# Kernel optimization log

Measured on AMD Instinct MI355X. Metric: run time of the kernel, lower is better.

## Reference

```python
import jax, jax.numpy as jnp
import numpy as np

N_NODES = 100000
N_EDGES = 1600000
N_GRAPHS = 2000
N_FEAT = 128
HIDDEN = 128
N_LAYERS = 4
BN_EPS = 1e-5


def setup_inputs() -> dict:
    key = jax.random.key(0)
    ks = jax.random.split(key, 8)
    x = jax.random.normal(ks[0], (N_NODES, N_FEAT), dtype=jnp.float32)
    edge_index = jax.random.randint(ks[1], (2, N_EDGES), 0, N_NODES, dtype=jnp.int32)
    batch = jnp.sort(jax.random.randint(ks[2], (N_NODES,), 0, N_GRAPHS, dtype=jnp.int32))
    # layer weights scaled down to keep activations stable over 4 layers
    Ws = jax.random.normal(ks[3], (N_LAYERS, HIDDEN, HIDDEN), dtype=jnp.float32) * 0.1
    bs = jnp.zeros((N_LAYERS, HIDDEN), jnp.float32)
    gammas = jnp.ones((N_LAYERS, HIDDEN), jnp.float32)
    betas = jnp.zeros((N_LAYERS, HIDDEN), jnp.float32)
    run_mean = jnp.zeros((N_LAYERS, HIDDEN), jnp.float32)
    run_var = jnp.ones((N_LAYERS, HIDDEN), jnp.float32)
    W_out = jax.random.normal(ks[4], (HIDDEN, 5), dtype=jnp.float32) * 0.1
    b_out = jnp.zeros((5,), jnp.float32)
    return {"x": x, "edge_index": edge_index, "batch": batch, "Ws": Ws, "bs": bs,
            "gammas": gammas, "betas": betas, "run_mean": run_mean, "run_var": run_var,
            "W_out": W_out, "b_out": b_out}


def _gcn_conv(x, src, dst, norm, self_coef, W, b):
    xw = x @ W                                        # [N, H]
    coef = norm[src] * norm[dst]                      # [E]
    msgs = xw[src] * coef[:, None]                    # [E, H] gather
    agg = jax.ops.segment_sum(msgs, dst, num_segments=N_NODES)  # scatter-add
    agg = agg + xw * self_coef[:, None]               # self-loop term
    return agg + b


def reference(x, edge_index, batch, Ws, bs, gammas, betas, run_mean, run_var, W_out, b_out):
    src, dst = edge_index[0], edge_index[1]
    # degree (incl. self-loop) from destination index
    deg = jax.ops.segment_sum(jnp.ones((N_EDGES,), x.dtype), dst, num_segments=N_NODES) + 1.0
    norm = jax.lax.rsqrt(deg)
    self_coef = norm * norm
    h = x
    for l in range(N_LAYERS):
        h = _gcn_conv(h, src, dst, norm, self_coef, Ws[l], bs[l])
        # BatchNorm1d in eval mode (running stats); dropout is identity in eval
        h = (h - run_mean[l]) * (gammas[l] * jax.lax.rsqrt(run_var[l] + BN_EPS)) + betas[l]
        h = jax.nn.relu(h)
    # global mean pool over graphs
    sums = jax.ops.segment_sum(h, batch, num_segments=N_GRAPHS)
    counts = jax.ops.segment_sum(jnp.ones((N_NODES,), h.dtype), batch, num_segments=N_GRAPHS)
    pooled = sums / jnp.maximum(counts, 1.0)[:, None]  # [G, H]
    return pooled @ W_out + b_out                      # [G, 5]
```

## Files before the change

kernel.cpp:

```cpp
#include <hip/hip_runtime.h>
#include <hip/hip_fp16.h>

#define N_NODES_C 100000
#define N_EDGES_C 1600000
#define N_GRAPHS_C 2000
#define HID 128
#define BN_EPS_C 1e-5f
#define NBUCK 391
#define PART_TILE 4096

typedef _Float16 half8 __attribute__((ext_vector_type(8)));
typedef float float4v __attribute__((ext_vector_type(4)));


__global__ __launch_bounds__(256) void kb_hist(const int* __restrict__ dst, int* __restrict__ bcount) {
    __shared__ int hist[NBUCK];
    const int t = threadIdx.x;
    for (int b = t; b < NBUCK; b += 256) hist[b] = 0;
    __syncthreads();
    const int e0 = blockIdx.x * PART_TILE;
    #pragma unroll
    for (int k = 0; k < 16; k++) {
        int e = e0 + k * 256 + t;
        if (e < N_EDGES_C) atomicAdd(&hist[dst[e] >> 8], 1);
    }
    __syncthreads();
    for (int b = t; b < NBUCK; b += 256) {
        int c = hist[b];
        if (c) atomicAdd(&bcount[b], c);
    }
}

__global__ __launch_bounds__(512) void kb_scan(const int* __restrict__ bcount,
                                               int* __restrict__ bbase, int* __restrict__ bcursor) {
    __shared__ int s[512];
    const int t = threadIdx.x;
    int v = (t < NBUCK) ? bcount[t] : 0;
    s[t] = v;
    __syncthreads();
    for (int off = 1; off < 512; off <<= 1) {
        int u = (t >= off) ? s[t - off] : 0;
        __syncthreads();
        s[t] += u;
        __syncthreads();
    }
    if (t < NBUCK) { int e = s[t] - v; bbase[t] = e; bcursor[t] = e; }
    if (t == 0) bbase[NBUCK] = N_EDGES_C;
}

__global__ __launch_bounds__(256) void kb_part(const int* __restrict__ src, const int* __restrict__ dst,
                                               int* __restrict__ bcursor, int2* __restrict__ ebuf) {
    __shared__ int hist[NBUCK];
    __shared__ int startA[NBUCK];
    __shared__ int lcur[NBUCK];
    const int t = threadIdx.x;
    for (int b = t; b < NBUCK; b += 256) { hist[b] = 0; lcur[b] = 0; }
    __syncthreads();
    const int e0 = blockIdx.x * PART_TILE;
    #pragma unroll
    for (int k = 0; k < 16; k++) {
        int e = e0 + k * 256 + t;
        if (e < N_EDGES_C) atomicAdd(&hist[dst[e] >> 8], 1);
    }
    __syncthreads();
    for (int b = t; b < NBUCK; b += 256) {
        int c = hist[b];
        startA[b] = c ? atomicAdd(&bcursor[b], c) : 0;
    }
    __syncthreads();
    #pragma unroll
    for (int k = 0; k < 16; k++) {
        int e = e0 + k * 256 + t;
        if (e < N_EDGES_C) {
            int d = dst[e];
            int b = d >> 8;
            int pos = startA[b] + atomicAdd(&lcur[b], 1);
            ebuf[pos] = make_int2(src[e], d);
        }
    }
}

__global__ __launch_bounds__(256) void kb_fill(const int2* __restrict__ ebuf, const int* __restrict__ bbase,
                                               int* __restrict__ csr_src, int* __restrict__ offs,
                                               float* __restrict__ norm) {
    __shared__ int s[256];
    __shared__ int excl[256];
    __shared__ int lcur[256];
    const int b = blockIdx.x, t = threadIdx.x;
    const int base = b << 8;
    const int e0 = bbase[b], e1 = bbase[b + 1];
    s[t] = 0; lcur[t] = 0;
    __syncthreads();
    for (int e = e0 + t; e < e1; e += 256)
        atomicAdd(&s[ebuf[e].y & 255], 1);
    __syncthreads();
    int own = s[t];
    for (int off = 1; off < 256; off <<= 1) {
        int v = (t >= off) ? s[t - off] : 0;
        __syncthreads();
        s[t] += v;
        __syncthreads();
    }
    excl[t] = s[t] - own;
    int node = base + t;
    if (node < N_NODES_C) {
        offs[node] = e0 + (s[t] - own);
        norm[node] = rsqrtf((float)own + 1.0f);
    }
    if (b == 0 && t == 0) offs[N_NODES_C] = N_EDGES_C;
    __syncthreads();
    for (int e = e0 + t; e < e1; e += 256) {
        int2 p = ebuf[e];
        int l = p.y & 255;
        int pos = e0 + excl[l] + atomicAdd(&lcur[l], 1);
        csr_src[pos] = p.x;
    }
}


__global__ __launch_bounds__(256) void k_cast(const float* __restrict__ x, _Float16* __restrict__ xh) {
    long i = ((long)blockIdx.x * 256 + threadIdx.x) * 8;
    float4 a = *(const float4*)&x[i];
    float4 b = *(const float4*)&x[i + 4];
    _Float16 p[8] = {(_Float16)a.x, (_Float16)a.y, (_Float16)a.z, (_Float16)a.w,
                     (_Float16)b.x, (_Float16)b.y, (_Float16)b.z, (_Float16)b.w};
    *(half8*)&xh[i] = *(half8*)p;
}

__global__ __launch_bounds__(256) void k_tw(const float* __restrict__ Ws_all, _Float16* __restrict__ WT) {
    int idx = blockIdx.x * 256 + threadIdx.x;
    int l = idx >> 14, r = idx & 16383, k = r >> 7, n = r & 127;
    WT[l * 16384 + n * HID + k] = (_Float16)Ws_all[idx];
}


__global__ __launch_bounds__(256) void k_gemm(const _Float16* __restrict__ Ah,
                                              const _Float16* __restrict__ WT,
                                              const float* __restrict__ norm,
                                              _Float16* __restrict__ Y, int nrows) {
    __shared__ _Float16 Wt[HID][136];
    const int tid = threadIdx.x;
    #pragma unroll
    for (int t = 0; t < 8; t++) {
        int off = tid * 8 + t * 2048;
        half8 v = *(const half8*)&WT[off];
        *(half8*)&Wt[off >> 7][off & 127] = v;
    }
    __syncthreads();

    const int wave = tid >> 6, lane = tid & 63, quad = lane >> 4, l16 = lane & 15;
    half8 Wf[2][4];
    #pragma unroll
    for (int c = 0; c < 2; c++)
        #pragma unroll
        for (int ks = 0; ks < 4; ks++)
            Wf[c][ks] = *(const half8*)&Wt[(wave * 2 + c) * 16 + l16][ks * 32 + quad * 8];

    const int nbase = blockIdx.x * 128;
    #pragma unroll
    for (int t = 0; t < 8; t++) {
        int node = nbase + t * 16 + l16;
        bool ok = node < nrows;
        half8 Af[4];
        const _Float16* arow = Ah + (long)node * HID;
        #pragma unroll
        for (int ks = 0; ks < 4; ks++)
            Af[ks] = ok ? *(const half8*)&arow[ks * 32 + quad * 8] : half8{};
        float4v a0 = {0.f, 0.f, 0.f, 0.f}, a1 = {0.f, 0.f, 0.f, 0.f};
        #pragma unroll
        for (int ks = 0; ks < 4; ks++) {
            a0 = __builtin_amdgcn_mfma_f32_16x16x32_f16(Wf[0][ks], Af[ks], a0, 0, 0, 0);
            a1 = __builtin_amdgcn_mfma_f32_16x16x32_f16(Wf[1][ks], Af[ks], a1, 0, 0, 0);
        }
        if (ok) {
            float nv = norm[node];
            _Float16 p0[4], p1[4];
            #pragma unroll
            for (int r = 0; r < 4; r++) {
                p0[r] = (_Float16)(a0[r] * nv);
                p1[r] = (_Float16)(a1[r] * nv);
            }
            *(ushort4*)&Y[(long)node * HID + (wave * 2 + 0) * 16 + quad * 4] = *(ushort4*)p0;
            *(ushort4*)&Y[(long)node * HID + (wave * 2 + 1) * 16 + quad * 4] = *(ushort4*)p1;
        }
    }
}


__global__ __launch_bounds__(256) void k_agg(const __half* __restrict__ y, const int* __restrict__ offs,
                                             const int* __restrict__ csr_src, const float* __restrict__ norm,
                                             const float* __restrict__ bias, const float* __restrict__ mean,
                                             const float* __restrict__ gamma, const float* __restrict__ var,
                                             const float* __restrict__ beta, __half* __restrict__ h) {
    const int wave = __builtin_amdgcn_readfirstlane(threadIdx.x >> 6);
    const int lane = threadIdx.x & 63;
    const int i = blockIdx.x * 4 + wave;
    const int j = lane * 2;

    float2 f = __half22float2(*(const __half2*)&y[(long)i * HID + j]);
    float acc0 = f.x, acc1 = f.y;

    const int e0 = offs[i], e1 = offs[i + 1];
    int e = e0;
    #define GATHER(EE) { \
        int s_ = csr_src[EE]; \
        float2 g_ = __half22float2(*(const __half2*)&y[(long)s_ * HID + j]); \
        acc0 += g_.x; acc1 += g_.y; }
    for (; e + 8 <= e1; e += 8) {
        GATHER(e) GATHER(e + 1) GATHER(e + 2) GATHER(e + 3)
        GATHER(e + 4) GATHER(e + 5) GATHER(e + 6) GATHER(e + 7)
    }
    for (; e < e1; e++) GATHER(e)
    #undef GATHER

    float ni = norm[i];
    float2 bi = *(const float2*)&bias[j];
    float2 me = *(const float2*)&mean[j];
    float2 ga = *(const float2*)&gamma[j];
    float2 va = *(const float2*)&var[j];
    float2 be = *(const float2*)&beta[j];
    float v0 = (acc0 * ni + bi.x - me.x) * (ga.x * rsqrtf(va.x + BN_EPS_C)) + be.x;
    float v1 = (acc1 * ni + bi.y - me.y) * (ga.y * rsqrtf(va.y + BN_EPS_C)) + be.y;
    *(__half2*)&h[(long)i * HID + j] = __floats2half2_rn(fmaxf(v0, 0.f), fmaxf(v1, 0.f));
}


__global__ __launch_bounds__(128) void k_pool(const __half* __restrict__ h, const int* __restrict__ batch,
                                              float* __restrict__ psum, int* __restrict__ pcount) {
    const int j = threadIdx.x;
    const int i0 = blockIdx.x * 128;
    const int iend = min(i0 + 128, N_NODES_C);
    if (i0 >= N_NODES_C) return;
    float acc = 0.f;
    int cur = batch[i0];
    int runStart = i0;
    for (int i = i0; i < iend; i++) {
        int g = batch[i];
        if (g != cur) {
            atomicAdd(&psum[(long)cur * HID + j], acc);
            if (j == 0) atomicAdd(&pcount[cur], i - runStart);
            acc = 0.f; cur = g; runStart = i;
        }
        acc += __half2float(h[(long)i * HID + j]);
    }
    atomicAdd(&psum[(long)cur * HID + j], acc);
    if (j == 0) atomicAdd(&pcount[cur], iend - runStart);
}

__global__ __launch_bounds__(128) void k_final(const float* __restrict__ psum, const int* __restrict__ pcount,
                                               const float* __restrict__ W_out, const float* __restrict__ b_out,
                                               float* __restrict__ out) {
    __shared__ float red[128][5];
    const int g = blockIdx.x, j = threadIdx.x;
    float cnt = fmaxf((float)pcount[g], 1.f);
    float p = psum[(long)g * HID + j] / cnt;
    #pragma unroll
    for (int o = 0; o < 5; o++) red[j][o] = p * W_out[j * 5 + o];
    __syncthreads();
    for (int off = 64; off >= 1; off >>= 1) {
        if (j < off) {
            #pragma unroll
            for (int o = 0; o < 5; o++) red[j][o] += red[j + off][o];
        }
        __syncthreads();
    }
    if (j < 5) out[g * 5 + j] = red[0][j] + b_out[j];
}


extern "C" void kernel_launch(void* const* d_in, const int* in_sizes, int n_in,
                              void* d_out, int out_size, void* d_ws, size_t ws_size,
                              hipStream_t stream) {
    const float* x        = (const float*)d_in[0];
    const int*   eidx     = (const int*)d_in[1];
    const int*   src      = eidx;
    const int*   dst      = eidx + N_EDGES_C;
    const int*   batch    = (const int*)d_in[2];
    const float* Ws_all   = (const float*)d_in[3];
    const float* bs       = (const float*)d_in[4];
    const float* gammas   = (const float*)d_in[5];
    const float* betas    = (const float*)d_in[6];
    const float* run_mean = (const float*)d_in[7];
    const float* run_var  = (const float*)d_in[8];
    const float* W_out    = (const float*)d_in[9];
    const float* b_out    = (const float*)d_in[10];
    float* out = (float*)d_out;

    char* wp = (char*)d_ws;
    auto alloc = [&](size_t bytes) { char* p = wp; wp += (bytes + 255) & ~(size_t)255; return p; };
    __half*   h       = (__half*)alloc((size_t)N_NODES_C * HID * 2);
    _Float16* y       = (_Float16*)alloc((size_t)N_NODES_C * HID * 2);
    int2*     ebuf    = (int2*)y;
    _Float16* xh      = (_Float16*)alloc((size_t)N_NODES_C * HID * 2);
    _Float16* WT      = (_Float16*)alloc((size_t)4 * HID * HID * 2);
    int*      csr_src = (int*)alloc((size_t)N_EDGES_C * 4);
    int*      offs    = (int*)alloc((size_t)(N_NODES_C + 1) * 4);
    float*    norm    = (float*)alloc((size_t)N_NODES_C * 4);
    int*      bcount  = (int*)alloc((NBUCK + 1) * 4);
    int*      bbase   = (int*)alloc((NBUCK + 1) * 4);
    int*      bcursor = (int*)alloc((NBUCK + 1) * 4);
    float*    psum    = (float*)alloc((size_t)N_GRAPHS_C * HID * 4);
    int*      pcount  = (int*)alloc((size_t)N_GRAPHS_C * 4);

    hipMemsetAsync(bcount, 0, (NBUCK + 1) * 4, stream);
    hipMemsetAsync(psum,   0, (size_t)N_GRAPHS_C * HID * 4, stream);
    hipMemsetAsync(pcount, 0, (size_t)N_GRAPHS_C * 4, stream);

    k_cast<<<(N_NODES_C * HID) / 2048, 256, 0, stream>>>(x, xh);
    k_tw  <<<256, 256, 0, stream>>>(Ws_all, WT);

    const int PB = (N_EDGES_C + PART_TILE - 1) / PART_TILE;
    kb_hist<<<PB, 256, 0, stream>>>(dst, bcount);
    kb_scan<<<1, 512, 0, stream>>>(bcount, bbase, bcursor);
    kb_part<<<PB, 256, 0, stream>>>(src, dst, bcursor, ebuf);
    kb_fill<<<NBUCK, 256, 0, stream>>>(ebuf, bbase, csr_src, offs, norm);

    const int GB = (N_NODES_C + 127) / 128;
    const int AB = (N_NODES_C + 3) / 4;
    for (int l = 0; l < 4; l++) {
        const _Float16* A = (l == 0) ? xh : (const _Float16*)h;
        k_gemm<<<GB, 256, 0, stream>>>(A, WT + (size_t)l * HID * HID, norm, y, N_NODES_C);
        k_agg<<<AB, 256, 0, stream>>>((const __half*)y, offs, csr_src, norm,
                                      bs + l * HID, run_mean + l * HID, gammas + l * HID,
                                      run_var + l * HID, betas + l * HID, h);
    }
    k_pool <<<GB, 128, 0, stream>>>(h, batch, psum, pcount);
    k_final<<<N_GRAPHS_C, 128, 0, stream>>>(psum, pcount, W_out, b_out, out);
}
```

Before: 555.5 us.

## Widen aggregation gathers, pack edge buffer, precompute BN affine, drop GEMM LDS staging

The aggregation kernel now has each 16-lane group load a full 16-byte half8 chunk per neighbor, with four edges handled in parallel per wave and combined by cross-lane shuffles. This replaces per-lane 4-byte gathers and is meant to cut memory transactions on the dominant gather. The edge partition buffer packs src and the low dst bits into one 32-bit word, halving that traffic. BatchNorm scale and shift are precomputed once per layer in a tiny kernel. The GEMM reads weights straight from global memory instead of staging them in LDS, and the pool kernel processes two columns per thread.

New measurement: 568.9 us. +2.4%, slower.

```diff
diff --git a/kernel.cpp b/kernel.cpp
--- a/kernel.cpp
+++ b/kernel.cpp
@@ -49,7 +49,7 @@
 }
 
 __global__ __launch_bounds__(256) void kb_part(const int* __restrict__ src, const int* __restrict__ dst,
-                                               int* __restrict__ bcursor, int2* __restrict__ ebuf) {
+                                               int* __restrict__ bcursor, unsigned int* __restrict__ ebuf) {
     __shared__ int hist[NBUCK];
     __shared__ int startA[NBUCK];
     __shared__ int lcur[NBUCK];
@@ -75,12 +75,12 @@
             int d = dst[e];
             int b = d >> 8;
             int pos = startA[b] + atomicAdd(&lcur[b], 1);
-            ebuf[pos] = make_int2(src[e], d);
-        }
-    }
-}
-
-__global__ __launch_bounds__(256) void kb_fill(const int2* __restrict__ ebuf, const int* __restrict__ bbase,
+            ebuf[pos] = ((unsigned int)src[e] << 8) | (unsigned int)(d & 255);
+        }
+    }
+}
+
+__global__ __launch_bounds__(256) void kb_fill(const unsigned int* __restrict__ ebuf, const int* __restrict__ bbase,
                                                int* __restrict__ csr_src, int* __restrict__ offs,
                                                float* __restrict__ norm) {
     __shared__ int s[256];
@@ -92,7 +92,7 @@
     s[t] = 0; lcur[t] = 0;
     __syncthreads();
     for (int e = e0 + t; e < e1; e += 256)
-        atomicAdd(&s[ebuf[e].y & 255], 1);
+        atomicAdd(&s[ebuf[e] & 255u], 1);
     __syncthreads();
     int own = s[t];
     for (int off = 1; off < 256; off <<= 1) {
@@ -110,21 +110,21 @@
     if (b == 0 && t == 0) offs[N_NODES_C] = N_EDGES_C;
     __syncthreads();
     for (int e = e0 + t; e < e1; e += 256) {
-        int2 p = ebuf[e];
-        int l = p.y & 255;
+        unsigned int p = ebuf[e];
+        int l = p & 255u;
         int pos = e0 + excl[l] + atomicAdd(&lcur[l], 1);
-        csr_src[pos] = p.x;
+        csr_src[pos] = (int)(p >> 8);
     }
 }
 
 
 __global__ __launch_bounds__(256) void k_cast(const float* __restrict__ x, _Float16* __restrict__ xh) {
-    long i = ((long)blockIdx.x * 256 + threadIdx.x) * 8;
-    float4 a = *(const float4*)&x[i];
-    float4 b = *(const float4*)&x[i + 4];
+    long base = ((long)blockIdx.x * 256 + threadIdx.x) * 8;
+    float4 a = *(const float4*)&x[base];
+    float4 b = *(const float4*)&x[base + 4];
     _Float16 p[8] = {(_Float16)a.x, (_Float16)a.y, (_Float16)a.z, (_Float16)a.w,
                      (_Float16)b.x, (_Float16)b.y, (_Float16)b.z, (_Float16)b.w};
-    *(half8*)&xh[i] = *(half8*)p;
+    *(half8*)&xh[base] = *(half8*)p;
 }
 
 __global__ __launch_bounds__(256) void k_tw(const float* __restrict__ Ws_all, _Float16* __restrict__ WT) {
@@ -133,28 +133,32 @@
     WT[l * 16384 + n * HID + k] = (_Float16)Ws_all[idx];
 }
 
+__global__ __launch_bounds__(256) void k_bn(const float* __restrict__ bs, const float* __restrict__ mean,
+                                            const float* __restrict__ gamma, const float* __restrict__ var,
+                                            const float* __restrict__ beta,
+                                            float* __restrict__ Asc, float* __restrict__ Bsh) {
+    int i = blockIdx.x * 256 + threadIdx.x;
+    if (i < 4 * HID) {
+        float sc = gamma[i] * rsqrtf(var[i] + BN_EPS_C);
+        Asc[i] = sc;
+        Bsh[i] = (bs[i] - mean[i]) * sc + beta[i];
+    }
+}
+
 
 __global__ __launch_bounds__(256) void k_gemm(const _Float16* __restrict__ Ah,
                                               const _Float16* __restrict__ WT,
                                               const float* __restrict__ norm,
                                               _Float16* __restrict__ Y, int nrows) {
-    __shared__ _Float16 Wt[HID][136];
     const int tid = threadIdx.x;
-    #pragma unroll
-    for (int t = 0; t < 8; t++) {
-        int off = tid * 8 + t * 2048;
-        half8 v = *(const half8*)&WT[off];
-        *(half8*)&Wt[off >> 7][off & 127] = v;
-    }
-    __syncthreads();
-
     const int wave = tid >> 6, lane = tid & 63, quad = lane >> 4, l16 = lane & 15;
+
     half8 Wf[2][4];
     #pragma unroll
     for (int c = 0; c < 2; c++)
         #pragma unroll
         for (int ks = 0; ks < 4; ks++)
-            Wf[c][ks] = *(const half8*)&Wt[(wave * 2 + c) * 16 + l16][ks * 32 + quad * 8];
+            Wf[c][ks] = *(const half8*)&WT[((wave * 2 + c) * 16 + l16) * HID + ks * 32 + quad * 8];
 
     const int nbase = blockIdx.x * 128;
     #pragma unroll
@@ -187,63 +191,98 @@
 }
 
 
-__global__ __launch_bounds__(256) void k_agg(const __half* __restrict__ y, const int* __restrict__ offs,
+__global__ __launch_bounds__(256) void k_agg(const _Float16* __restrict__ y, const int* __restrict__ offs,
                                              const int* __restrict__ csr_src, const float* __restrict__ norm,
-                                             const float* __restrict__ bias, const float* __restrict__ mean,
-                                             const float* __restrict__ gamma, const float* __restrict__ var,
-                                             const float* __restrict__ beta, __half* __restrict__ h) {
-    const int wave = __builtin_amdgcn_readfirstlane(threadIdx.x >> 6);
+                                             const float* __restrict__ Asc, const float* __restrict__ Bsh,
+                                             _Float16* __restrict__ h) {
+    const int wave = threadIdx.x >> 6;
     const int lane = threadIdx.x & 63;
+    const int q = lane >> 4, cl = lane & 15;
     const int i = blockIdx.x * 4 + wave;
-    const int j = lane * 2;
-
-    float2 f = __half22float2(*(const __half2*)&y[(long)i * HID + j]);
-    float acc0 = f.x, acc1 = f.y;
+
+    float acc[8] = {0.f, 0.f, 0.f, 0.f, 0.f, 0.f, 0.f, 0.f};
+    if (q == 0) {
+        half8 sv = *(const half8*)&y[(long)i * HID + cl * 8];
+        #pragma unroll
+        for (int r = 0; r < 8; r++) acc[r] += (float)sv[r];
+    }
 
     const int e0 = offs[i], e1 = offs[i + 1];
     int e = e0;
-    #define GATHER(EE) { \
-        int s_ = csr_src[EE]; \
-        float2 g_ = __half22float2(*(const __half2*)&y[(long)s_ * HID + j]); \
-        acc0 += g_.x; acc1 += g_.y; }
-    for (; e + 8 <= e1; e += 8) {
-        GATHER(e) GATHER(e + 1) GATHER(e + 2) GATHER(e + 3)
-        GATHER(e + 4) GATHER(e + 5) GATHER(e + 6) GATHER(e + 7)
-    }
-    for (; e < e1; e++) GATHER(e)
-    #undef GATHER
-
-    float ni = norm[i];
-    float2 bi = *(const float2*)&bias[j];
-    float2 me = *(const float2*)&mean[j];
-    float2 ga = *(const float2*)&gamma[j];
-    float2 va = *(const float2*)&var[j];
-    float2 be = *(const float2*)&beta[j];
-    float v0 = (acc0 * ni + bi.x - me.x) * (ga.x * rsqrtf(va.x + BN_EPS_C)) + be.x;
-    float v1 = (acc1 * ni + bi.y - me.y) * (ga.y * rsqrtf(va.y + BN_EPS_C)) + be.y;
-    *(__half2*)&h[(long)i * HID + j] = __floats2half2_rn(fmaxf(v0, 0.f), fmaxf(v1, 0.f));
-}
-
-
-__global__ __launch_bounds__(128) void k_pool(const __half* __restrict__ h, const int* __restrict__ batch,
-                                              float* __restrict__ psum, int* __restrict__ pcount) {
+    for (; e + 16 <= e1; e += 16) {
+        int s0 = csr_src[e + q];
+        int s1 = csr_src[e + 4 + q];
+        int s2 = csr_src[e + 8 + q];
+        int s3 = csr_src[e + 12 + q];
+        half8 v0 = *(const half8*)&y[(long)s0 * HID + cl * 8];
+        half8 v1 = *(const half8*)&y[(long)s1 * HID + cl * 8];
+        half8 v2 = *(const half8*)&y[(long)s2 * HID + cl * 8];
+        half8 v3 = *(const half8*)&y[(long)s3 * HID + cl * 8];
+        #pragma unroll
+        for (int r = 0; r < 8; r++)
+            acc[r] += (float)v0[r] + (float)v1[r] + (float)v2[r] + (float)v3[r];
+    }
+    for (; e + 4 <= e1; e += 4) {
+        int s = csr_src[e + q];
+        half8 v = *(const half8*)&y[(long)s * HID + cl * 8];
+        #pragma unroll
+        for (int r = 0; r < 8; r++) acc[r] += (float)v[r];
+    }
+    if (e + q < e1) {
+        int s = csr_src[e + q];
+        half8 v = *(const half8*)&y[(long)s * HID + cl * 8];
+        #pragma unroll
+        for (int r = 0; r < 8; r++) acc[r] += (float)v[r];
+    }
+
+    #pragma unroll
+    for (int r = 0; r < 8; r++) {
+        acc[r] += __shfl_xor(acc[r], 16);
+        acc[r] += __shfl_xor(acc[r], 32);
+    }
+
+    if (q == 0) {
+        float ni = norm[i];
+        float4 A0 = *(const float4*)&Asc[cl * 8];
+        float4 A1 = *(const float4*)&Asc[cl * 8 + 4];
+        float4 B0 = *(const float4*)&Bsh[cl * 8];
+        float4 B1 = *(const float4*)&Bsh[cl * 8 + 4];
+        _Float16 p[8];
+        p[0] = (_Float16)fmaxf(acc[0] * ni * A0.x + B0.x, 0.f);
+        p[1] = (_Float16)fmaxf(acc[1] * ni * A0.y + B0.y, 0.f);
+        p[2] = (_Float16)fmaxf(acc[2] * ni * A0.z + B0.z, 0.f);
+        p[3] = (_Float16)fmaxf(acc[3] * ni * A0.w + B0.w, 0.f);
+        p[4] = (_Float16)fmaxf(acc[4] * ni * A1.x + B1.x, 0.f);
+        p[5] = (_Float16)fmaxf(acc[5] * ni * A1.y + B1.y, 0.f);
+        p[6] = (_Float16)fmaxf(acc[6] * ni * A1.z + B1.z, 0.f);
+        p[7] = (_Float16)fmaxf(acc[7] * ni * A1.w + B1.w, 0.f);
+        *(half8*)&h[(long)i * HID + cl * 8] = *(half8*)p;
+    }
+}
+
+
+__global__ __launch_bounds__(64) void k_pool(const __half* __restrict__ h, const int* __restrict__ batch,
+                                             float* __restrict__ psum, int* __restrict__ pcount) {
     const int j = threadIdx.x;
     const int i0 = blockIdx.x * 128;
     const int iend = min(i0 + 128, N_NODES_C);
     if (i0 >= N_NODES_C) return;
-    float acc = 0.f;
+    float acc0 = 0.f, acc1 = 0.f;
     int cur = batch[i0];
     int runStart = i0;
     for (int i = i0; i < iend; i++) {
-        int g = batch[i];
-        if (g != cur) {
-            atomicAdd(&psum[(long)cur * HID + j], acc);
+        int gidx = batch[i];
+        if (gidx != cur) {
+            atomicAdd(&psum[(long)cur * HID + 2 * j], acc0);
+            atomicAdd(&psum[(long)cur * HID + 2 * j + 1], acc1);
             if (j == 0) atomicAdd(&pcount[cur], i - runStart);
-            acc = 0.f; cur = g; runStart = i;
-        }
-        acc += __half2float(h[(long)i * HID + j]);
-    }
-    atomicAdd(&psum[(long)cur * HID + j], acc);
+            acc0 = 0.f; acc1 = 0.f; cur = gidx; runStart = i;
+        }
+        float2 f = __half22float2(*(const __half2*)&h[(long)i * HID + 2 * j]);
+        acc0 += f.x; acc1 += f.y;
+    }
+    atomicAdd(&psum[(long)cur * HID + 2 * j], acc0);
+    atomicAdd(&psum[(long)cur * HID + 2 * j + 1], acc1);
     if (j == 0) atomicAdd(&pcount[cur], iend - runStart);
 }
 
@@ -288,11 +327,13 @@
 
     char* wp = (char*)d_ws;
     auto alloc = [&](size_t bytes) { char* p = wp; wp += (bytes + 255) & ~(size_t)255; return p; };
-    __half*   h       = (__half*)alloc((size_t)N_NODES_C * HID * 2);
+    _Float16* xh      = (_Float16*)alloc((size_t)N_NODES_C * HID * 2);
     _Float16* y       = (_Float16*)alloc((size_t)N_NODES_C * HID * 2);
-    int2*     ebuf    = (int2*)y;
-    _Float16* xh      = (_Float16*)alloc((size_t)N_NODES_C * HID * 2);
+    unsigned int* ebuf = (unsigned int*)y;
+    _Float16* h       = (_Float16*)alloc((size_t)N_NODES_C * HID * 2);
     _Float16* WT      = (_Float16*)alloc((size_t)4 * HID * HID * 2);
+    float*    Asc     = (float*)alloc((size_t)4 * HID * 4);
+    float*    Bsh     = (float*)alloc((size_t)4 * HID * 4);
     int*      csr_src = (int*)alloc((size_t)N_EDGES_C * 4);
     int*      offs    = (int*)alloc((size_t)(N_NODES_C + 1) * 4);
     float*    norm    = (float*)alloc((size_t)N_NODES_C * 4);
@@ -306,24 +347,24 @@
     hipMemsetAsync(psum,   0, (size_t)N_GRAPHS_C * HID * 4, stream);
     hipMemsetAsync(pcount, 0, (size_t)N_GRAPHS_C * 4, stream);
 
-    k_cast<<<(N_NODES_C * HID) / 2048, 256, 0, stream>>>(x, xh);
-    k_tw  <<<256, 256, 0, stream>>>(Ws_all, WT);
-
     const int PB = (N_EDGES_C + PART_TILE - 1) / PART_TILE;
     kb_hist<<<PB, 256, 0, stream>>>(dst, bcount);
     kb_scan<<<1, 512, 0, stream>>>(bcount, bbase, bcursor);
     kb_part<<<PB, 256, 0, stream>>>(src, dst, bcursor, ebuf);
     kb_fill<<<NBUCK, 256, 0, stream>>>(ebuf, bbase, csr_src, offs, norm);
 
+    k_tw  <<<256, 256, 0, stream>>>(Ws_all, WT);
+    k_bn  <<<2, 256, 0, stream>>>(bs, run_mean, gammas, run_var, betas, Asc, Bsh);
+    k_cast<<<(N_NODES_C * HID) / 2048, 256, 0, stream>>>(x, xh);
+
     const int GB = (N_NODES_C + 127) / 128;
     const int AB = (N_NODES_C + 3) / 4;
     for (int l = 0; l < 4; l++) {
-        const _Float16* A = (l == 0) ? xh : (const _Float16*)h;
+        const _Float16* A = (l == 0) ? xh : h;
         k_gemm<<<GB, 256, 0, stream>>>(A, WT + (size_t)l * HID * HID, norm, y, N_NODES_C);
-        k_agg<<<AB, 256, 0, stream>>>((const __half*)y, offs, csr_src, norm,
-                                      bs + l * HID, run_mean + l * HID, gammas + l * HID,
-                                      run_var + l * HID, betas + l * HID, h);
-    }
-    k_pool <<<GB, 128, 0, stream>>>(h, batch, psum, pcount);
+        k_agg<<<AB, 256, 0, stream>>>(y, offs, csr_src, norm,
+                                      Asc + l * HID, Bsh + l * HID, h);
+    }
+    k_pool <<<GB, 64, 0, stream>>>((const __half*)h, batch, psum, pcount);
     k_final<<<N_GRAPHS_C, 128, 0, stream>>>(psum, pcount, W_out, b_out, out);
 }
```
